# Performance work log

Measured on AMD Instinct MI355X. Metric: run time of the kernel, lower is better.

## Reference

```python
import jax, jax.numpy as jnp
import numpy as np

B, C, S, OUT = 64, 3, 448, 224


def setup_inputs() -> dict:
    key = jax.random.key(0)
    k1, k2 = jax.random.split(key)
    images = jax.random.normal(k1, (B, C, S, S), dtype=jnp.float32)
    # locs = sigmoid(apn) * in_size in the original model -> uniform in [0, S]
    locs = jax.random.uniform(k2, (B, 3), dtype=jnp.float32) * S
    return {"images": images, "locs": locs}


def _crop_resize(images, locs):
    # Faithful batched version of AttentionCropFunction.forward.
    b, c, s, _ = images.shape
    fS = jnp.float32(s)
    tx, ty, tl = locs[:, 0], locs[:, 1], locs[:, 2]
    # per-sample clamping exactly as the python if-chains
    tl = jnp.clip(tl, fS / 3.0, fS * 2.0 / 3.0)
    tx = jnp.clip(tx, tl, fS - tl)
    ty = jnp.clip(ty, tl, fS - tl)
    # int() truncation; args are >= 0 here so floor == trunc
    w_off = jnp.maximum(jnp.floor(tx - tl), 0.0)
    w_end = jnp.where(tx + tl < fS, jnp.floor(tx + tl), fS)
    h_off = jnp.maximum(jnp.floor(ty - tl), 0.0)
    h_end = jnp.where(ty + tl < fS, jnp.floor(ty + tl), fS)

    # soft box mask: h(v) = sigmoid(10 v); x grid varies along rows (dim -2),
    # y grid along cols (dim -1), matching unit.t() / unit in the original.
    coords = jnp.arange(s, dtype=jnp.float32)
    sig = jax.nn.sigmoid
    mrow = sig(10.0 * (coords[None, :] - w_off[:, None])) - sig(10.0 * (coords[None, :] - w_end[:, None]))  # [B,S]
    mcol = sig(10.0 * (coords[None, :] - h_off[:, None])) - sig(10.0 * (coords[None, :] - h_end[:, None]))  # [B,S]
    masked = images * mrow[:, None, :, None] * mcol[:, None, None, :]  # [B,C,S,S]

    def axis_src(off, end):
        # bilinear upsample of slice [off:end] to OUT with align_corners=True:
        # output index r samples absolute input coord off + r*(L-1)/(OUT-1)
        L = end - off  # crop length (integer-valued float)
        r = jnp.arange(OUT, dtype=jnp.float32)
        return off[:, None] + r[None, :] * (L[:, None] - 1.0) / (OUT - 1.0)  # [B,OUT]

    def interp_axis(x, src, axis):
        # linear interpolation of x along `axis` (2 or 3) at positions src [B,OUT]
        i0 = jnp.clip(jnp.floor(src), 0.0, s - 1.0).astype(jnp.int32)
        i1 = jnp.clip(i0 + 1, 0, s - 1)
        fr = src - i0.astype(jnp.float32)
        shp = [src.shape[0], 1, 1, 1]
        shp[axis] = OUT
        tgt = x.shape[:axis] + (OUT,) + x.shape[axis + 1:]
        g0 = jnp.take_along_axis(x, jnp.broadcast_to(i0.reshape(shp), tgt), axis=axis)
        g1 = jnp.take_along_axis(x, jnp.broadcast_to(i1.reshape(shp), tgt), axis=axis)
        frb = fr.reshape(shp)
        return g0 * (1.0 - frb) + g1 * frb

    rows = interp_axis(masked, axis_src(w_off, w_end), 2)  # [B,C,OUT,S]
    out = interp_axis(rows, axis_src(h_off, h_end), 3)     # [B,C,OUT,OUT]
    return out


def reference(images, locs):
    return _crop_resize(images, locs)
```

## Files before the change

### kernel.cpp

```cpp
#include <hip/hip_runtime.h>


#define B_N 64
#define C_N 3
#define S_N 448
#define O_N 224
#define BLOCK 256

__device__ __forceinline__ float sigm(float x) {
    return 1.0f / (1.0f + __expf(-x));
}

__global__ __launch_bounds__(BLOCK) void racnn_crop_resize(
    const float* __restrict__ images,
    const float* __restrict__ locs,
    float* __restrict__ out) {
    __shared__ float comb[C_N][S_N];

    const int r = blockIdx.x;
    const int b = blockIdx.y;
    const int tid = threadIdx.x;

    const float fS = (float)S_N;

    float tx = locs[b * 3 + 0];
    float ty = locs[b * 3 + 1];
    float tl = locs[b * 3 + 2];
    tl = fminf(fmaxf(tl, fS / 3.0f), fS * (2.0f / 3.0f));
    tx = fminf(fmaxf(tx, tl), fS - tl);
    ty = fminf(fmaxf(ty, tl), fS - tl);

    float w_off = fmaxf(floorf(tx - tl), 0.0f);
    float w_end = (tx + tl < fS) ? floorf(tx + tl) : fS;
    float h_off = fmaxf(floorf(ty - tl), 0.0f);
    float h_end = (ty + tl < fS) ? floorf(ty + tl) : fS;

    float src_r = w_off + (float)r * (w_end - w_off - 1.0f) * (1.0f / (float)(O_N - 1));
    float f0r = fminf(fmaxf(floorf(src_r), 0.0f), fS - 1.0f);
    int i0r = (int)f0r;
    int i1r = min(i0r + 1, S_N - 1);
    float frr = src_r - f0r;
    float mr0 = sigm(10.0f * (f0r - w_off)) - sigm(10.0f * (f0r - w_end));
    float mr1 = sigm(10.0f * ((float)i1r - w_off)) - sigm(10.0f * ((float)i1r - w_end));
    float A  = mr0 * (1.0f - frr);
    float Bw = mr1 * frr;

    int col_lo = (int)h_off;
    int col_hi = min((int)h_end, S_N - 1);
    int W = col_hi - col_lo + 1;

    const size_t plane = (size_t)S_N * S_N;
    const float* base = images + (size_t)b * C_N * plane;
#pragma unroll
    for (int c = 0; c < C_N; ++c) {
        const float* p0 = base + c * plane + (size_t)i0r * S_N;
        const float* p1 = base + c * plane + (size_t)i1r * S_N;
        for (int j = col_lo + tid; j <= col_hi; j += BLOCK) {
            comb[c][j - col_lo] = p0[j] * A + p1[j] * Bw;
        }
    }
    __syncthreads();

    if (tid < O_N) {
        const int q = tid;
        float src_q = h_off + (float)q * (h_end - h_off - 1.0f) * (1.0f / (float)(O_N - 1));
        float f0q = fminf(fmaxf(floorf(src_q), 0.0f), fS - 1.0f);
        int i0q = (int)f0q;
        int i1q = min(i0q + 1, S_N - 1);
        float frq = src_q - f0q;
        float mq0 = sigm(10.0f * (f0q - h_off)) - sigm(10.0f * (f0q - h_end));
        float mq1 = sigm(10.0f * ((float)i1q - h_off)) - sigm(10.0f * ((float)i1q - h_end));

        int x0 = min(max(i0q - col_lo, 0), W - 1);
        int x1 = min(max(i1q - col_lo, 0), W - 1);
        float wa = mq0 * (1.0f - frq);
        float wb = mq1 * frq;

#pragma unroll
        for (int c = 0; c < C_N; ++c) {
            float o = comb[c][x0] * wa + comb[c][x1] * wb;
            out[(((size_t)b * C_N + c) * O_N + r) * O_N + q] = o;
        }
    }
}

extern "C" void kernel_launch(void* const* d_in, const int* in_sizes, int n_in,
                              void* d_out, int out_size, void* d_ws, size_t ws_size,
                              hipStream_t stream) {
    const float* images = (const float*)d_in[0];
    const float* locs   = (const float*)d_in[1];
    float* out = (float*)d_out;

    dim3 grid(O_N, B_N);
    racnn_crop_resize<<<grid, BLOCK, 0, stream>>>(images, locs, out);
}
```

Measured before the change: 38.08 us.

## Process four output rows per block with 448 threads to cut per-block overhead

Each block now handles four output rows instead of one, using 448 threads so each thread loads one column for all four rows and three channels. The second pass lets all 448 threads work, each writing two rows, instead of leaving 32 of 256 idle. This cuts the block count and amortizes the per-block locs and clamp setup. It also adds independent loads per thread. The costs are fewer blocks (3584), larger shared memory per block and more registers, which may lower occupancy. Source rows shared between adjacent output rows are not deduplicated.

Measured after the change: 42.47 us. +11.5%, slower.

```diff
diff --git a/kernel.cpp b/kernel.cpp
--- a/kernel.cpp
+++ b/kernel.cpp
@@ -5,7 +5,8 @@
 #define C_N 3
 #define S_N 448
 #define O_N 224
-#define BLOCK 256
+#define BLOCK 448
+#define RPB 4
 
 __device__ __forceinline__ float sigm(float x) {
     return 1.0f / (1.0f + __expf(-x));
@@ -15,9 +16,9 @@
     const float* __restrict__ images,
     const float* __restrict__ locs,
     float* __restrict__ out) {
-    __shared__ float comb[C_N][S_N];
+    __shared__ float comb[RPB][C_N][S_N];
 
-    const int r = blockIdx.x;
+    const int r0 = blockIdx.x * RPB;
     const int b = blockIdx.y;
     const int tid = threadIdx.x;
 
@@ -35,50 +36,68 @@
     float h_off = fmaxf(floorf(ty - tl), 0.0f);
     float h_end = (ty + tl < fS) ? floorf(ty + tl) : fS;
 
-    float src_r = w_off + (float)r * (w_end - w_off - 1.0f) * (1.0f / (float)(O_N - 1));
-    float f0r = fminf(fmaxf(floorf(src_r), 0.0f), fS - 1.0f);
-    int i0r = (int)f0r;
-    int i1r = min(i0r + 1, S_N - 1);
-    float frr = src_r - f0r;
-    float mr0 = sigm(10.0f * (f0r - w_off)) - sigm(10.0f * (f0r - w_end));
-    float mr1 = sigm(10.0f * ((float)i1r - w_off)) - sigm(10.0f * ((float)i1r - w_end));
-    float A  = mr0 * (1.0f - frr);
-    float Bw = mr1 * frr;
+    const int col_lo = (int)h_off;
+    const int col_hi = min((int)h_end, S_N - 1);
 
-    int col_lo = (int)h_off;
-    int col_hi = min((int)h_end, S_N - 1);
-    int W = col_hi - col_lo + 1;
+    int i0r_[RPB], i1r_[RPB];
+    float Ar[RPB], Br[RPB];
+    const float inv_o1 = 1.0f / (float)(O_N - 1);
+#pragma unroll
+    for (int rr = 0; rr < RPB; ++rr) {
+        float src_r = w_off + (float)(r0 + rr) * (w_end - w_off - 1.0f) * inv_o1;
+        float f0r = fminf(fmaxf(floorf(src_r), 0.0f), fS - 1.0f);
+        int i0r = (int)f0r;
+        int i1r = min(i0r + 1, S_N - 1);
+        float frr = src_r - f0r;
+        float mr0 = sigm(10.0f * (f0r - w_off)) - sigm(10.0f * (f0r - w_end));
+        float mr1 = sigm(10.0f * ((float)i1r - w_off)) - sigm(10.0f * ((float)i1r - w_end));
+        i0r_[rr] = i0r;
+        i1r_[rr] = i1r;
+        Ar[rr] = mr0 * (1.0f - frr);
+        Br[rr] = mr1 * frr;
+    }
 
     const size_t plane = (size_t)S_N * S_N;
     const float* base = images + (size_t)b * C_N * plane;
+    const int j = col_lo + tid;
+    if (j <= col_hi) {
 #pragma unroll
-    for (int c = 0; c < C_N; ++c) {
-        const float* p0 = base + c * plane + (size_t)i0r * S_N;
-        const float* p1 = base + c * plane + (size_t)i1r * S_N;
-        for (int j = col_lo + tid; j <= col_hi; j += BLOCK) {
-            comb[c][j - col_lo] = p0[j] * A + p1[j] * Bw;
+        for (int rr = 0; rr < RPB; ++rr) {
+            const float* p0 = base + (size_t)i0r_[rr] * S_N;
+            const float* p1 = base + (size_t)i1r_[rr] * S_N;
+            float a = Ar[rr], bb = Br[rr];
+#pragma unroll
+            for (int c = 0; c < C_N; ++c) {
+                comb[rr][c][tid] = p0[c * plane + j] * a + p1[c * plane + j] * bb;
+            }
         }
     }
     __syncthreads();
 
-    if (tid < O_N) {
-        const int q = tid;
-        float src_q = h_off + (float)q * (h_end - h_off - 1.0f) * (1.0f / (float)(O_N - 1));
-        float f0q = fminf(fmaxf(floorf(src_q), 0.0f), fS - 1.0f);
-        int i0q = (int)f0q;
-        int i1q = min(i0q + 1, S_N - 1);
-        float frq = src_q - f0q;
-        float mq0 = sigm(10.0f * (f0q - h_off)) - sigm(10.0f * (f0q - h_end));
-        float mq1 = sigm(10.0f * ((float)i1q - h_off)) - sigm(10.0f * ((float)i1q - h_end));
+    const int q = tid % O_N;
+    const int half = tid / O_N;
 
-        int x0 = min(max(i0q - col_lo, 0), W - 1);
-        int x1 = min(max(i1q - col_lo, 0), W - 1);
-        float wa = mq0 * (1.0f - frq);
-        float wb = mq1 * frq;
+    float src_q = h_off + (float)q * (h_end - h_off - 1.0f) * inv_o1;
+    float f0q = fminf(fmaxf(floorf(src_q), 0.0f), fS - 1.0f);
+    int i0q = (int)f0q;
+    int i1q = min(i0q + 1, S_N - 1);
+    float frq = src_q - f0q;
+    float mq0 = sigm(10.0f * (f0q - h_off)) - sigm(10.0f * (f0q - h_end));
+    float mq1 = sigm(10.0f * ((float)i1q - h_off)) - sigm(10.0f * ((float)i1q - h_end));
+
+    const int W = col_hi - col_lo + 1;
+    int x0 = min(max(i0q - col_lo, 0), W - 1);
+    int x1 = min(max(i1q - col_lo, 0), W - 1);
+    float wa = mq0 * (1.0f - frq);
+    float wb = mq1 * frq;
 
 #pragma unroll
+    for (int rr = 0; rr < 2; ++rr) {
+        const int r_local = half + 2 * rr;
+        const int r = r0 + r_local;
+#pragma unroll
         for (int c = 0; c < C_N; ++c) {
-            float o = comb[c][x0] * wa + comb[c][x1] * wb;
+            float o = comb[r_local][c][x0] * wa + comb[r_local][c][x1] * wb;
             out[(((size_t)b * C_N + c) * O_N + r) * O_N + q] = o;
         }
     }
@@ -91,6 +110,6 @@
     const float* locs   = (const float*)d_in[1];
     float* out = (float*)d_out;
 
-    dim3 grid(O_N, B_N);
+    dim3 grid(O_N / RPB, B_N);
     racnn_crop_resize<<<grid, BLOCK, 0, stream>>>(images, locs, out);
 }
```

## Vectorize row loads to float4 and remap blocks for XCD locality

Applied to the files above, without the earlier changes.

The row-gather phase now reads both source rows as aligned float4 loads over a 4-aligned column range and flattens the channel loop into a single strided loop. The grid becomes 1D, and block IDs are remapped so that consecutive logical rows of the same batch land on the same XCD, which improves L2 reuse of shared source rows. The trade-offs are a slightly wider loaded column range plus padded shared memory, and some extra index arithmetic per block.

Result: faster. 33.14 us (-13.0%).

```diff
diff --git a/kernel.cpp b/kernel.cpp
--- a/kernel.cpp
+++ b/kernel.cpp
@@ -6,6 +6,8 @@
 #define S_N 448
 #define O_N 224
 #define BLOCK 256
+#define NXCD 8
+#define NV_PAD 113
 
 __device__ __forceinline__ float sigm(float x) {
     return 1.0f / (1.0f + __expf(-x));
@@ -15,10 +17,12 @@
     const float* __restrict__ images,
     const float* __restrict__ locs,
     float* __restrict__ out) {
-    __shared__ float comb[C_N][S_N];
+    __shared__ float4 comb4[C_N][NV_PAD];
 
-    const int r = blockIdx.x;
-    const int b = blockIdx.y;
+    const int bid = blockIdx.x;
+    const int logical = (bid % NXCD) * (O_N * B_N / NXCD) + bid / NXCD;
+    const int r = logical % O_N;
+    const int b = logical / O_N;
     const int tid = threadIdx.x;
 
     const float fS = (float)S_N;
@@ -35,35 +39,48 @@
     float h_off = fmaxf(floorf(ty - tl), 0.0f);
     float h_end = (ty + tl < fS) ? floorf(ty + tl) : fS;
 
-    float src_r = w_off + (float)r * (w_end - w_off - 1.0f) * (1.0f / (float)(O_N - 1));
+    const float inv_o1 = 1.0f / (float)(O_N - 1);
+
+    float src_r = w_off + (float)r * (w_end - w_off - 1.0f) * inv_o1;
     float f0r = fminf(fmaxf(floorf(src_r), 0.0f), fS - 1.0f);
     int i0r = (int)f0r;
     int i1r = min(i0r + 1, S_N - 1);
     float frr = src_r - f0r;
     float mr0 = sigm(10.0f * (f0r - w_off)) - sigm(10.0f * (f0r - w_end));
     float mr1 = sigm(10.0f * ((float)i1r - w_off)) - sigm(10.0f * ((float)i1r - w_end));
-    float A  = mr0 * (1.0f - frr);
-    float Bw = mr1 * frr;
+    const float A  = mr0 * (1.0f - frr);
+    const float Bw = mr1 * frr;
 
-    int col_lo = (int)h_off;
-    int col_hi = min((int)h_end, S_N - 1);
-    int W = col_hi - col_lo + 1;
+    const int col_lo = (int)h_off;
+    const int col_hi = min((int)h_end, S_N - 1);
+    const int c4lo = col_lo >> 2;
+    const int nv = (col_hi >> 2) - c4lo + 1;
 
-    const size_t plane = (size_t)S_N * S_N;
-    const float* base = images + (size_t)b * C_N * plane;
-#pragma unroll
-    for (int c = 0; c < C_N; ++c) {
-        const float* p0 = base + c * plane + (size_t)i0r * S_N;
-        const float* p1 = base + c * plane + (size_t)i1r * S_N;
-        for (int j = col_lo + tid; j <= col_hi; j += BLOCK) {
-            comb[c][j - col_lo] = p0[j] * A + p1[j] * Bw;
-        }
+    const float4* img4 = reinterpret_cast<const float4*>(images);
+    const size_t plane4 = (size_t)(S_N * S_N / 4);
+    const size_t row4 = S_N / 4;
+    const size_t base4 = (size_t)b * C_N * plane4;
+    const size_t off0 = (size_t)i0r * row4 + c4lo;
+    const size_t off1 = (size_t)i1r * row4 + c4lo;
+
+    const int total = C_N * nv;
+    for (int v = tid; v < total; v += BLOCK) {
+        int c = (v >= nv) + (v >= 2 * nv);
+        int j4 = v - c * nv;
+        const float4 a = img4[base4 + (size_t)c * plane4 + off0 + j4];
+        const float4 bb = img4[base4 + (size_t)c * plane4 + off1 + j4];
+        float4 o;
+        o.x = a.x * A + bb.x * Bw;
+        o.y = a.y * A + bb.y * Bw;
+        o.z = a.z * A + bb.z * Bw;
+        o.w = a.w * A + bb.w * Bw;
+        comb4[c][j4] = o;
     }
     __syncthreads();
 
     if (tid < O_N) {
         const int q = tid;
-        float src_q = h_off + (float)q * (h_end - h_off - 1.0f) * (1.0f / (float)(O_N - 1));
+        float src_q = h_off + (float)q * (h_end - h_off - 1.0f) * inv_o1;
         float f0q = fminf(fmaxf(floorf(src_q), 0.0f), fS - 1.0f);
         int i0q = (int)f0q;
         int i1q = min(i0q + 1, S_N - 1);
@@ -71,14 +88,18 @@
         float mq0 = sigm(10.0f * (f0q - h_off)) - sigm(10.0f * (f0q - h_end));
         float mq1 = sigm(10.0f * ((float)i1q - h_off)) - sigm(10.0f * ((float)i1q - h_end));
 
-        int x0 = min(max(i0q - col_lo, 0), W - 1);
-        int x1 = min(max(i1q - col_lo, 0), W - 1);
+        const int wlim = nv * 4 - 1;
+        const int base_col = c4lo << 2;
+        int x0 = min(max(i0q - base_col, 0), wlim);
+        int x1 = min(max(i1q - base_col, 0), wlim);
         float wa = mq0 * (1.0f - frq);
         float wb = mq1 * frq;
 
+        const float* combf = reinterpret_cast<const float*>(comb4);
 #pragma unroll
         for (int c = 0; c < C_N; ++c) {
-            float o = comb[c][x0] * wa + comb[c][x1] * wb;
+            float o = combf[c * (NV_PAD * 4) + x0] * wa +
+                      combf[c * (NV_PAD * 4) + x1] * wb;
             out[(((size_t)b * C_N + c) * O_N + r) * O_N + q] = o;
         }
     }
@@ -91,6 +112,5 @@
     const float* locs   = (const float*)d_in[1];
     float* out = (float*)d_out;
 
-    dim3 grid(O_N, B_N);
-    racnn_crop_resize<<<grid, BLOCK, 0, stream>>>(images, locs, out);
+    racnn_crop_resize<<<O_N * B_N, BLOCK, 0, stream>>>(images, locs, out);
 }
```
